# Performance work log

Hardware: AMD Instinct MI355X
Metric: run time of the kernel (lower is better)

## Reference

```python
import jax, jax.numpy as jnp
import numpy as np

N_VERTS = 200000
N_TETS = 800000
FREQ_NUM = 4
SCALE = 1.0
HID = 256
D_IN = 3 + 6 * FREQ_NUM  # 27

_TRI_TABLE = np.array([
    [-1,-1,-1,-1,-1,-1],[1,0,2,-1,-1,-1],[4,0,3,-1,-1,-1],[1,4,2,1,3,4],
    [3,1,5,-1,-1,-1],[2,3,0,2,5,3],[1,4,0,1,5,4],[4,2,5,-1,-1,-1],
    [4,5,2,-1,-1,-1],[4,1,0,4,5,1],[3,2,0,3,5,2],[1,3,5,-1,-1,-1],
    [4,1,2,4,3,1],[3,0,4,-1,-1,-1],[2,0,1,-1,-1,-1],[-1,-1,-1,-1,-1,-1]], dtype=np.int32)
_NUM_TRI = np.array([0,1,1,2,1,2,2,1,1,2,2,1,2,1,1,0], dtype=np.int32)
_BASE_EDGES = np.array([0,1,0,2,0,3,1,2,1,3,2,3], dtype=np.int32)


def _pos_enc(x):
    feats = [x]
    for i in range(FREQ_NUM):
        f = float(2 ** i) * np.pi / SCALE
        feats.append(jnp.sin(f * x))
        feats.append(jnp.cos(f * x))
    return jnp.concatenate(feats, axis=-1)  # [N, 27]


def _mlp_sdf(pos, w0, b0, w1, b1, w2, b2, w3, b3, wf, bf):
    h = jax.nn.relu(_pos_enc(pos) @ w0 + b0)
    for w, b in ((w1, b1), (w2, b2), (w3, b3)):
        h = jax.nn.relu(h @ w + b)
    return (h @ wf + bf)[:, 0]  # [N]


def setup_inputs() -> dict:
    key = jax.random.key(0)
    ks = jax.random.split(key, 12)
    def lin(k, fan_in, shape):
        return jax.random.normal(k, shape, jnp.float32) * (2.0 / fan_in) ** 0.5
    return {
        "pos": jax.random.normal(ks[0], (N_VERTS, 3), jnp.float32),
        "tet_fx4": jax.random.randint(ks[1], (N_TETS, 4), 0, N_VERTS, dtype=jnp.int32),
        "w0": lin(ks[2], D_IN, (D_IN, HID)), "b0": jnp.zeros((HID,), jnp.float32),
        "w1": lin(ks[3], HID, (HID, HID)), "b1": jnp.zeros((HID,), jnp.float32),
        "w2": lin(ks[4], HID, (HID, HID)), "b2": jnp.zeros((HID,), jnp.float32),
        "w3": lin(ks[5], HID, (HID, HID)), "b3": jnp.zeros((HID,), jnp.float32),
        "wf": lin(ks[6], HID, (HID, 1)), "bf": jnp.zeros((1,), jnp.float32),
    }


def reference(pos, tet_fx4, w0, b0, w1, b1, w2, b2, w3, b3, wf, bf):
    # SDF from the positional-encoding MLP (DMTetGeometry)
    sdf = _mlp_sdf(pos, w0, b0, w1, b1, w2, b2, w3, b3, wf, bf)

    # --- marching tetrahedra (DMTet.__call__) ---
    occ = sdf > 0                       # [N]
    occ_fx4 = occ[tet_fx4]              # [F,4]
    occ_sum = occ_fx4.sum(-1)
    valid = (occ_sum > 0) & (occ_sum < 4)
    vt = tet_fx4[valid]                 # [V,4] tets crossed by the surface
    occ_v = occ_fx4[valid]              # [V,4]

    # all 6 edges per valid tet, sorted so (lo, hi)
    e = vt[:, _BASE_EDGES].reshape(-1, 2)                         # [6V,2]
    e = jnp.stack([jnp.minimum(e[:, 0], e[:, 1]),
                   jnp.maximum(e[:, 0], e[:, 1])], axis=1)
    uniq, inv = jnp.unique(e, axis=0, return_inverse=True)        # dedup edges
    inv = inv.reshape(-1)

    # edges whose endpoints straddle the zero level set
    cross = occ[uniq].sum(-1) == 1                                 # [U]
    mapping = jnp.where(cross, jnp.cumsum(cross) - 1, -1)          # compact ids
    idx_map = mapping[inv].reshape(-1, 6)                          # [V,6]
    interp_v = uniq[cross]                                         # [M,2]

    # linear interpolation of crossing vertices along each crossing edge
    p = pos[interp_v]                                              # [M,2,3]
    s = sdf[interp_v]                                              # [M,2]
    denom = s[:, 0] - s[:, 1]                                      # s0 + (-s1)
    verts = (p[:, 0] * (-s[:, 1])[:, None] + p[:, 1] * s[:, 0][:, None]) / denom[:, None]

    # triangle table lookup
    tetindex = (occ_v.astype(jnp.int32) * (2 ** jnp.arange(4, dtype=jnp.int32))).sum(-1)
    ntri = jnp.asarray(_NUM_TRI)[tetindex]
    tri = jnp.asarray(_TRI_TABLE)[tetindex]
    m1 = ntri == 1
    m2 = ntri == 2
    f1 = jnp.take_along_axis(idx_map[m1], tri[m1][:, :3], axis=1).reshape(-1, 3)
    f2 = jnp.take_along_axis(idx_map[m2], tri[m2][:, :6], axis=1).reshape(-1, 3)
    faces = jnp.concatenate([f1, f2], axis=0)
    return verts, faces
```

## Files before the change

kernel.cpp:

```cpp
#include <hip/hip_runtime.h>
#include <cstdint>
#include <cstddef>

#define NV 200000
#define NT 800000
#define ROWS 64
#define MBLK 3125
#define NBLK 3125
#define NSEGS 196
#define PCAP 4096

typedef unsigned int u32;
typedef unsigned long long u64;

typedef __attribute__((ext_vector_type(8))) _Float16 half8;
typedef __attribute__((ext_vector_type(4))) float f32x4;
#define MFMA16F __builtin_amdgcn_mfma_f32_16x16x32_f16

__constant__ int c_tri[16][6] = {
  {-1,-1,-1,-1,-1,-1},{1,0,2,-1,-1,-1},{4,0,3,-1,-1,-1},{1,4,2,1,3,4},
  {3,1,5,-1,-1,-1},{2,3,0,2,5,3},{1,4,0,1,5,4},{4,2,5,-1,-1,-1},
  {4,5,2,-1,-1,-1},{4,1,0,4,5,1},{3,2,0,3,5,2},{1,3,5,-1,-1,-1},
  {4,1,2,4,3,1},{3,0,4,-1,-1,-1},{2,0,1,-1,-1,-1},{-1,-1,-1,-1,-1,-1}};
__constant__ int c_ntri[16] = {0,1,1,2,1,2,2,1,1,2,2,1,2,1,1,0};
__constant__ int c_be[12] = {0,1,0,2,0,3,1,2,1,3,2,3};

__device__ __forceinline__ void split2(float x, _Float16& h, _Float16& m){
  h = (_Float16)x;
  const float r = x - (float)h;
  m = (_Float16)(r * 2048.0f);
}

__global__ void split_weights(const float* __restrict__ w0, const float* __restrict__ w1,
                              const float* __restrict__ w2, const float* __restrict__ w3,
                              _Float16* __restrict__ wp, u32* __restrict__ segcur)
{
  const int idx = blockIdx.x*256 + threadIdx.x;
  if (idx < 256) segcur[idx] = 0u;
  int base, k, n, psz;
  float val;
  if (idx < 8192){
    base = 0; psz = 8192; k = idx >> 8; n = idx & 255;
    val = (k < 27) ? w0[k*256 + n] : 0.f;
  } else {
    int r = idx - 8192;
    const int l = r >> 16;
    r &= 65535;
    k = r >> 8; n = r & 255; psz = 65536;
    base = 16384 + l*131072;
    const float* w = (l==0) ? w1 : (l==1) ? w2 : w3;
    val = w[k*256 + n];
  }
  _Float16 h, m; split2(val, h, m);
  const int c = k >> 5, kk = k & 31;
  const int off = (c*256 + n)*32 + kk;
  wp[base + off] = h;
  wp[base + psz + off] = m;
}

template<int NC, bool LAST>
__device__ __forceinline__ void layer_run(
    const _Float16* __restrict__ Wl, const float* __restrict__ Bv,
    const float* __restrict__ wfv,
    _Float16 (*Af)[ROWS][264], float (*part)[8],
    int lane, int wv)
{
  const int l15 = lane & 15, q = lane >> 4;
  const int col0 = wv * 32;
  f32x4 g0[4][2], g1[4][2];
#pragma unroll
  for (int i=0;i<4;i++)
#pragma unroll
    for (int j=0;j<2;j++){ g0[i][j] = (f32x4){0.f,0.f,0.f,0.f}; g1[i][j] = (f32x4){0.f,0.f,0.f,0.f}; }

  const _Float16* bp = Wl + (u32)((col0 + l15)*32 + q*8);
  half8 bA[2][2], bB[2][2];

  auto loadB = [&](int c, half8 (*dst)[2]){
#pragma unroll
    for (int p=0;p<2;p++)
#pragma unroll
      for (int nt=0;nt<2;nt++)
        dst[p][nt] = *(const half8*)(bp + (p*NC + c)*8192 + nt*512);
  };
  auto compute = [&](int c, const half8 (*bb)[2]){
#pragma unroll
    for (int mt=0;mt<4;mt++){
      const _Float16* ap = &Af[0][mt*16 + l15][c*32 + q*8];
      const half8 ah = *(const half8*)(ap);
      const half8 am = *(const half8*)(ap + ROWS*264);
#pragma unroll
      for (int nt=0;nt<2;nt++){
        g0[mt][nt] = MFMA16F(ah, bb[0][nt], g0[mt][nt], 0,0,0);
        g1[mt][nt] = MFMA16F(ah, bb[1][nt], g1[mt][nt], 0,0,0);
        g1[mt][nt] = MFMA16F(am, bb[0][nt], g1[mt][nt], 0,0,0);
      }
    }
  };

  loadB(0, bA);
  if (NC == 1){
    compute(0, bA);
  } else {
#pragma unroll 1
    for (int ch=0; ch<NC/2; ch++){
      const int c0 = 2*ch;
      loadB(c0+1, bB);
      compute(c0, bA);
      if (c0+2 < NC) loadB(c0+2, bA);
      compute(c0+1, bB);
    }
  }
  __syncthreads();

  const float S = 4.8828125e-4f;
  if (!LAST){
#pragma unroll
    for (int nt=0;nt<2;nt++){
      const int col = col0 + nt*16 + l15;
      const float bias = Bv[col];
#pragma unroll
      for (int mt=0;mt<4;mt++)
#pragma unroll
        for (int reg=0;reg<4;reg++){
          const int row = mt*16 + q*4 + reg;
          const float v = fmaxf(g0[mt][nt][reg] + S*g1[mt][nt][reg] + bias, 0.f);
          _Float16 h,m; split2(v,h,m);
          Af[0][row][col] = h; Af[1][row][col] = m;
        }
    }
  } else {
    float pr[4][4];
#pragma unroll
    for (int mt=0;mt<4;mt++)
#pragma unroll
      for (int reg=0;reg<4;reg++) pr[mt][reg] = 0.f;
#pragma unroll
    for (int nt=0;nt<2;nt++){
      const int col = col0 + nt*16 + l15;
      const float bias = Bv[col];
      const float w = wfv[col];
#pragma unroll
      for (int mt=0;mt<4;mt++)
#pragma unroll
        for (int reg=0;reg<4;reg++)
          pr[mt][reg] += fmaxf(g0[mt][nt][reg] + S*g1[mt][nt][reg] + bias, 0.f) * w;
    }
#pragma unroll
    for (int s=1;s<16;s<<=1)
#pragma unroll
      for (int mt=0;mt<4;mt++)
#pragma unroll
        for (int reg=0;reg<4;reg++)
          pr[mt][reg] += __shfl_xor(pr[mt][reg], s, 64);
    if (l15 == 0){
#pragma unroll
      for (int mt=0;mt<4;mt++)
#pragma unroll
        for (int reg=0;reg<4;reg++)
          part[mt*16 + q*4 + reg][wv] = pr[mt][reg];
    }
  }
  __syncthreads();
}

__global__ __launch_bounds__(512,4) void mlp_mfma(
    const float* __restrict__ pos, const _Float16* __restrict__ wp,
    const float* __restrict__ b0, const float* __restrict__ b1,
    const float* __restrict__ b2, const float* __restrict__ b3,
    const float* __restrict__ wf, const float* __restrict__ bf,
    float* __restrict__ sdf)
{
  __shared__ _Float16 Af[2][ROWS][264];
  __shared__ float part[ROWS][8];
  const int tid = threadIdx.x;
  const int lane = tid & 63, wv = tid >> 6;
  const int row0 = blockIdx.x * ROWS;

#pragma unroll
  for (int it=0; it<4; it++){
    const int idx = it*512 + tid;
    const int r = idx & 63, f = idx >> 6;
    float val = 0.f;
    if (f < 3){
      val = pos[(row0 + r)*3 + f];
    } else if (f < 27){
      const int g = (f-3)/6, rem = (f-3)%6;
      const int d = rem % 3;
      const float x = pos[(row0 + r)*3 + d];
      const float fr = (float)(1 << g) * 3.14159265358979323846f;
      val = (rem < 3) ? sinf(fr*x) : cosf(fr*x);
    }
    _Float16 h,m; split2(val,h,m);
    Af[0][r][f] = h; Af[1][r][f] = m;
  }
  __syncthreads();

  layer_run<1,false>(wp + 0,      b0, nullptr, Af, part, lane, wv);
  layer_run<8,false>(wp + 16384,  b1, nullptr, Af, part, lane, wv);
  layer_run<8,false>(wp + 147456, b2, nullptr, Af, part, lane, wv);
  layer_run<8,true >(wp + 278528, b3, wf,      Af, part, lane, wv);

  if (tid < ROWS){
    float s = 0.f;
#pragma unroll
    for (int w=0; w<8; w++) s += part[tid][w];
    sdf[row0 + tid] = s + bf[0];
  }
}

__device__ __forceinline__ u32 wave_scan_incl(u32 v, int lane){
#pragma unroll
  for (int s=1;s<64;s<<=1){
    const u32 y = __shfl_up(v, s, 64);
    if (lane >= s) v += y;
  }
  return v;
}
__device__ __forceinline__ u32 block_scan_fast(u32 v, u32* sh4, int tid){
  const int lane = tid & 63, wv = tid >> 6;
  const u32 incl = wave_scan_incl(v, lane);
  if (lane == 63) sh4[wv] = incl;
  __syncthreads();
  u32 base = 0;
#pragma unroll
  for (int w=0;w<3;w++) if (w < wv) base += sh4[w];
  return incl + base;
}
__device__ __forceinline__ u64 bscan_u64(u64 v, u64* sh, int tid){
  sh[tid]=v; __syncthreads();
#pragma unroll
  for (int s=1;s<256;s<<=1){
    const u64 y = (tid>=s) ? sh[tid-s] : 0ull;
    __syncthreads();
    sh[tid] += y;
    __syncthreads();
  }
  return sh[tid];
}

__global__ void tet_pairs(const int* __restrict__ tet, const float* __restrict__ sdf,
    unsigned char* __restrict__ codes, u32* __restrict__ tscan, u32* __restrict__ tsum,
    u32* __restrict__ segcur, u64* __restrict__ pairs)
{
  __shared__ u32 sh4[4];
  const int tid = threadIdx.x;
  const int t = blockIdx.x*256 + tid;
  const int4 v = *(const int4*)(&tet[4*t]);
  const int o0 = sdf[v.x] > 0.f;
  const int o1 = sdf[v.y] > 0.f;
  const int o2 = sdf[v.z] > 0.f;
  const int o3 = sdf[v.w] > 0.f;
  const int code = o0 | (o1<<1) | (o2<<2) | (o3<<3);
  codes[t] = (unsigned char)code;
  const int nt = c_ntri[code];
  if (nt > 0){
    const int vv[4] = {v.x, v.y, v.z, v.w};
    const int oc[4] = {o0,o1,o2,o3};
#pragma unroll
    for (int e=0;e<6;e++){
      const int ia = c_be[2*e], ib = c_be[2*e+1];
      if (oc[ia] != oc[ib]){
        const int p = vv[ia], q = vv[ib];
        const int lo = p<q ? p : q, hi = p<q ? q : p;
        const int seg = lo >> 10;
        const u32 slot = atomicAdd(&segcur[seg], 1u);
        if (slot < PCAP)
          pairs[(size_t)seg*PCAP + slot] = ((u64)(u32)lo << 32) | (u32)hi;
      }
    }
  }
  const u32 my = (u32)(nt==1) | ((u32)(nt==2)<<16);
  const u32 incl = block_scan_fast(my, sh4, tid);
  tscan[t] = incl - my;
  if (tid == 255) tsum[blockIdx.x] = incl;
}

__global__ void seg_process(const u64* __restrict__ pairs_in, const u32* __restrict__ segcur,
    u64* __restrict__ uq, u32* __restrict__ ucnt, u32* __restrict__ ucnt_ex,
    u32* __restrict__ usum, const u32* __restrict__ tsum, u64* __restrict__ tsumE,
    u32* __restrict__ meta)
{
  const int tid = threadIdx.x;
  if (blockIdx.x == NSEGS){
    __shared__ u64 sh64[256];
    u64 loc[13]; u64 tot = 0ull;
#pragma unroll
    for (int i=0;i<13;i++){
      const int idx = tid*13 + i;
      const u32 p = (idx < NBLK) ? tsum[idx] : 0u;
      const u64 u = (u64)(p & 0xffffu) | ((u64)(p >> 16) << 32);
      loc[i] = u; tot += u;
    }
    const u64 incl = bscan_u64(tot, sh64, tid);
    u64 run = incl - tot;
#pragma unroll
    for (int i=0;i<13;i++){
      const int idx = tid*13 + i;
      if (idx < NBLK) tsumE[idx] = run;
      run += loc[i];
    }
    if (tid == 255){ meta[0] = (u32)(incl & 0xffffffffull); meta[1] = (u32)(incl >> 32); }
    return;
  }

  __shared__ u64 P[PCAP];
  __shared__ u32 sh4[4];
  __shared__ u32 shbase;
  const int seg = blockIdx.x;
  int n = (int)segcur[seg];
  if (n > PCAP) n = PCAP;
  int np = 1; while (np < n) np <<= 1;

  for (int i=tid; i<np; i+=256)
    P[i] = (i < n) ? pairs_in[(size_t)seg*PCAP + i] : ~0ull;
  if (tid == 0) shbase = 0u;
  __syncthreads();

  for (int k=2; k<=np; k<<=1){
    for (int j=k>>1; j>0; j>>=1){
      for (int i=tid; i<np; i+=256){
        const int ij = i ^ j;
        if (ij > i){
          const u64 a = P[i], b = P[ij];
          const bool up = ((i & k) == 0);
          if ((a > b) == up){ P[i] = b; P[ij] = a; }
        }
      }
      __syncthreads();
    }
  }

  for (int c=0; c<n; c+=256){
    const int i = c + tid;
    u64 key = 0ull; u32 f = 0u;
    if (i < n){
      key = P[i];
      f = (i == 0 || P[i] != P[i-1]) ? 1u : 0u;
    }
    __syncthreads();
    const u32 incl = block_scan_fast(f, sh4, tid);
    const u32 base = shbase;
    if (f) P[base + incl - 1u] = key;
    __syncthreads();
    if (tid == 255) shbase = base + incl;
    __syncthreads();
  }
  const int uc = (int)shbase;

  for (int i=tid; i<uc; i+=256) uq[(size_t)seg*PCAP + i] = P[i];

  const int lo0 = seg << 10;
  for (int c=0; c<1024; c+=256){
    const int lo = lo0 + c + tid;
    if (lo < NV){
      const u64 kl = (u64)(u32)lo << 32;
      const u64 kh = (u64)(u32)(lo+1) << 32;
      int a=0, b=uc;
      while (a < b){ const int m=(a+b)>>1; if (P[m] < kl) a=m+1; else b=m; }
      const int lb = a;
      b = uc;
      while (a < b){ const int m=(a+b)>>1; if (P[m] < kh) a=m+1; else b=m; }
      ucnt_ex[lo] = (u32)lb;
      ucnt[lo] = (u32)(a - lb);
    }
  }
  if (tid == 0) usum[seg] = (u32)uc;
}

__global__ void emit_all(const int* __restrict__ tet, const float* __restrict__ pos,
    const float* __restrict__ sdf, const unsigned char* __restrict__ codes,
    const u32* __restrict__ tscan, const u64* __restrict__ tsumE, const u32* __restrict__ meta,
    const u64* __restrict__ uq, const u32* __restrict__ ucnt, const u32* __restrict__ ucnt_ex,
    const u32* __restrict__ usum, float* __restrict__ out, int out_size)
{
  __shared__ u32 sh4[4];
  __shared__ u32 shu[NSEGS];
  __shared__ u32 shM;
  const int tid = threadIdx.x;
  {
    const u32 v = (tid < NSEGS) ? usum[tid] : 0u;
    const u32 incl = block_scan_fast(v, sh4, tid);
    if (tid < NSEGS) shu[tid] = incl - v;
    if (tid == NSEGS-1) shM = incl;
    __syncthreads();
  }

  if (blockIdx.x < NSEGS){
    const int seg = blockIdx.x;
    const int uc = (int)usum[seg];
    const u32 base = shu[seg];
    for (int i=tid; i<uc; i+=256){
      const u64 key = uq[(size_t)seg*PCAP + i];
      const int lo = (int)(key >> 32);
      const int hi = (int)(key & 0xffffffffull);
      const float s0 = sdf[lo], s1 = sdf[hi];
      const float d = s0 - s1;
      const float vx = (pos[3*lo  ]*(-s1) + pos[3*hi  ]*s0) / d;
      const float vy = (pos[3*lo+1]*(-s1) + pos[3*hi+1]*s0) / d;
      const float vz = (pos[3*lo+2]*(-s1) + pos[3*hi+2]*s0) / d;
      const long long w = 3ll*(long long)(base + (u32)i);
      if (w + 3 <= (long long)out_size){
        out[w] = vx; out[w+1] = vy; out[w+2] = vz;
      }
    }
  } else {
    const int t = (blockIdx.x - NSEGS)*256 + tid;
    const int code = codes[t];
    const int nt = c_ntri[code];
    if (nt == 0) return;
    const u64 tb = tsumE[t>>8];
    const u32 ts = tscan[t];
    const u32 n1e = (u32)(tb & 0xffffffffull) + (ts & 0xffffu);
    const u32 n2e = (u32)(tb >> 32) + (ts >> 16);
    const u32 N1 = meta[0];
    const u32 M  = shM;
    const u32 fb = (nt==1) ? n1e : (N1 + 2u*n2e);
    const int4 v = *(const int4*)(&tet[4*t]);
    const int vv[4] = {v.x, v.y, v.z, v.w};
    for (int r=0;r<nt;r++){
      for (int k=0;k<3;k++){
        const int e = c_tri[code][3*r+k];
        const int ia = c_be[2*e], ib = c_be[2*e+1];
        const int p = vv[ia], q = vv[ib];
        const int lo = p<q ? p : q, hi = p<q ? q : p;
        const int seg = lo >> 10;
        const u32 st = ucnt_ex[lo];
        const int u = (int)ucnt[lo];
        const u64* b = uq + (size_t)seg*PCAP + st;
        int id = -1;
        for (int j=0;j<u;j++){
          if ((int)(b[j] & 0xffffffffull) == hi){ id = (int)(shu[seg] + st) + j; break; }
        }
        const long long w = 3ll*(long long)M + 3ll*(long long)(fb + (u32)r) + k;
        if (w < (long long)out_size && id >= 0) out[w] = (float)id;
      }
    }
  }
}

extern "C" void kernel_launch(void* const* d_in, const int* in_sizes, int n_in,
                              void* d_out, int out_size, void* d_ws, size_t ws_size,
                              hipStream_t stream)
{
  (void)in_sizes; (void)n_in; (void)ws_size;
  const float* pos = (const float*)d_in[0];
  const int*   tet = (const int*)d_in[1];
  const float* w0 = (const float*)d_in[2];
  const float* b0 = (const float*)d_in[3];
  const float* w1 = (const float*)d_in[4];
  const float* b1 = (const float*)d_in[5];
  const float* w2 = (const float*)d_in[6];
  const float* b2 = (const float*)d_in[7];
  const float* w3 = (const float*)d_in[8];
  const float* b3 = (const float*)d_in[9];
  const float* wf = (const float*)d_in[10];
  const float* bf = (const float*)d_in[11];
  float* out = (float*)d_out;
  char* ws = (char*)d_ws;

  float*         sdf   = (float*)(ws + 0);
  unsigned char* codes = (unsigned char*)(ws + 800000);
  u32* tscan   = (u32*)(ws + 1600000);
  u32* tsum    = (u32*)(ws + 4800000);
  u64* tsumE   = (u64*)(ws + 4812800);
  u32* segcur  = (u32*)(ws + 4837888);
  u32* usum    = (u32*)(ws + 4838912);
  u32* meta    = (u32*)(ws + 4839936);
  u32* ucnt    = (u32*)(ws + 4840000);
  u32* ucnt_ex = (u32*)(ws + 5640000);
  _Float16* wp = (_Float16*)(ws + 6440000);
  u64* pairs   = (u64*)(ws + 7259200);

  split_weights<<<800,256,0,stream>>>(w0,w1,w2,w3,wp,segcur);
  mlp_mfma<<<MBLK,512,0,stream>>>(pos,wp,b0,b1,b2,b3,wf,bf,sdf);

  tet_pairs<<<NBLK,256,0,stream>>>(tet,sdf,codes,tscan,tsum,segcur,pairs);
  seg_process<<<NSEGS+1,256,0,stream>>>(pairs,segcur,pairs,ucnt,ucnt_ex,usum,tsum,tsumE,meta);
  emit_all<<<NSEGS+NBLK,256,0,stream>>>(tet,pos,sdf,codes,tscan,tsumE,meta,
                                        pairs,ucnt,ucnt_ex,usum,out,out_size);
}
```

Measured before the change: 455.4 us.

## Replace per-layer block barriers with per-chunk progress flags and ping-pong activation buffers

The MLP kernel now keeps two ping-pong LDS activation buffers. Each wave publishes a per-column-chunk progress flag after writing its outputs, so consumers spin-wait only on the chunk they need instead of hitting a full __syncthreads between layers. Waves also start on staggered K chunks, and the LDS layout is XOR-swizzled to reduce bank conflicts. The aim is to cut barrier stalls between layers. In exchange, the doubled LDS use lowers occupancy (launch bounds drop from 4 to 2 blocks), and the flag polling adds spin overhead.

```diff
diff --git a/kernel.cpp b/kernel.cpp
--- a/kernel.cpp
+++ b/kernel.cpp
@@ -9,6 +9,8 @@
 #define NBLK 3125
 #define NSEGS 196
 #define PCAP 4096
+#define AST 264
+#define PST (ROWS*AST)
 
 typedef unsigned int u32;
 typedef unsigned long long u64;
@@ -58,15 +60,24 @@
   wp[base + psz + off] = m;
 }
 
+__device__ __forceinline__ void waitflag(u32* prog, int c, u32 epoch){
+  if (epoch == 0u) return;
+  while (__hip_atomic_load(&prog[c], __ATOMIC_ACQUIRE, __HIP_MEMORY_SCOPE_WORKGROUP) < epoch)
+    __builtin_amdgcn_s_sleep(1);
+}
+
 template<int NC, bool LAST>
 __device__ __forceinline__ void layer_run(
     const _Float16* __restrict__ Wl, const float* __restrict__ Bv,
     const float* __restrict__ wfv,
-    _Float16 (*Af)[ROWS][264], float (*part)[8],
+    const _Float16* __restrict__ Ain, _Float16* __restrict__ Aout,
+    float (*part)[9], u32* prog, u32 epoch,
     int lane, int wv)
 {
   const int l15 = lane & 15, q = lane >> 4;
   const int col0 = wv * 32;
+  const int rx  = ((l15 >> 3) & 1) << 4;
+  const int q8x = (q * 8) ^ rx;
   f32x4 g0[4][2], g1[4][2];
 #pragma unroll
   for (int i=0;i<4;i++)
@@ -86,9 +97,9 @@
   auto compute = [&](int c, const half8 (*bb)[2]){
 #pragma unroll
     for (int mt=0;mt<4;mt++){
-      const _Float16* ap = &Af[0][mt*16 + l15][c*32 + q*8];
+      const _Float16* ap = Ain + (u32)((mt*16 + l15)*AST + c*32 + q8x);
       const half8 ah = *(const half8*)(ap);
-      const half8 am = *(const half8*)(ap + ROWS*264);
+      const half8 am = *(const half8*)(ap + PST);
 #pragma unroll
       for (int nt=0;nt<2;nt++){
         g0[mt][nt] = MFMA16F(ah, bb[0][nt], g0[mt][nt], 0,0,0);
@@ -98,27 +109,31 @@
     }
   };
 
-  loadB(0, bA);
   if (NC == 1){
+    loadB(0, bA);
     compute(0, bA);
   } else {
+    loadB(wv & (NC-1), bA);
 #pragma unroll 1
     for (int ch=0; ch<NC/2; ch++){
-      const int c0 = 2*ch;
-      loadB(c0+1, bB);
-      compute(c0, bA);
-      if (c0+2 < NC) loadB(c0+2, bA);
-      compute(c0+1, bB);
-    }
-  }
-  __syncthreads();
+      const int cA = (wv + 2*ch)     & (NC-1);
+      const int cB = (wv + 2*ch + 1) & (NC-1);
+      loadB(cB, bB);
+      waitflag(prog, cA, epoch);
+      compute(cA, bA);
+      if (2*ch+2 < NC) loadB((wv + 2*ch + 2) & (NC-1), bA);
+      waitflag(prog, cB, epoch);
+      compute(cB, bB);
+    }
+  }
 
   const float S = 4.8828125e-4f;
   if (!LAST){
+    const int cx = ((q >> 1) & 1) << 4;
 #pragma unroll
     for (int nt=0;nt<2;nt++){
-      const int col = col0 + nt*16 + l15;
-      const float bias = Bv[col];
+      const int colb = ((col0 + nt*16) ^ cx) + l15;
+      const float bias = Bv[col0 + nt*16 + l15];
 #pragma unroll
       for (int mt=0;mt<4;mt++)
 #pragma unroll
@@ -126,9 +141,12 @@
           const int row = mt*16 + q*4 + reg;
           const float v = fmaxf(g0[mt][nt][reg] + S*g1[mt][nt][reg] + bias, 0.f);
           _Float16 h,m; split2(v,h,m);
-          Af[0][row][col] = h; Af[1][row][col] = m;
+          Aout[row*AST + colb] = h;
+          Aout[PST + row*AST + colb] = m;
         }
     }
+    if (lane == 0)
+      __hip_atomic_store(&prog[wv], epoch + 1u, __ATOMIC_RELEASE, __HIP_MEMORY_SCOPE_WORKGROUP);
   } else {
     float pr[4][4];
 #pragma unroll
@@ -161,21 +179,23 @@
           part[mt*16 + q*4 + reg][wv] = pr[mt][reg];
     }
   }
-  __syncthreads();
-}
-
-__global__ __launch_bounds__(512,4) void mlp_mfma(
+}
+
+__global__ __launch_bounds__(512,2) void mlp_mfma(
     const float* __restrict__ pos, const _Float16* __restrict__ wp,
     const float* __restrict__ b0, const float* __restrict__ b1,
     const float* __restrict__ b2, const float* __restrict__ b3,
     const float* __restrict__ wf, const float* __restrict__ bf,
     float* __restrict__ sdf)
 {
-  __shared__ _Float16 Af[2][ROWS][264];
-  __shared__ float part[ROWS][8];
+  __shared__ _Float16 Ab0[2*PST];
+  __shared__ _Float16 Ab1[2*PST];
+  __shared__ float part[ROWS][9];
+  __shared__ u32 prog[8];
   const int tid = threadIdx.x;
   const int lane = tid & 63, wv = tid >> 6;
   const int row0 = blockIdx.x * ROWS;
+  if (tid < 8) prog[tid] = 0u;
 
 #pragma unroll
   for (int it=0; it<4; it++){
@@ -192,14 +212,17 @@
       val = (rem < 3) ? sinf(fr*x) : cosf(fr*x);
     }
     _Float16 h,m; split2(val,h,m);
-    Af[0][r][f] = h; Af[1][r][f] = m;
+    const int fS = f ^ (((r >> 3) & 1) << 4);
+    Ab0[r*AST + fS] = h;
+    Ab0[PST + r*AST + fS] = m;
   }
   __syncthreads();
 
-  layer_run<1,false>(wp + 0,      b0, nullptr, Af, part, lane, wv);
-  layer_run<8,false>(wp + 16384,  b1, nullptr, Af, part, lane, wv);
-  layer_run<8,false>(wp + 147456, b2, nullptr, Af, part, lane, wv);
-  layer_run<8,true >(wp + 278528, b3, wf,      Af, part, lane, wv);
+  layer_run<1,false>(wp + 0,      b0, nullptr, Ab0, Ab1, part, prog, 0u, lane, wv);
+  layer_run<8,false>(wp + 16384,  b1, nullptr, Ab1, Ab0, part, prog, 1u, lane, wv);
+  layer_run<8,false>(wp + 147456, b2, nullptr, Ab0, Ab1, part, prog, 2u, lane, wv);
+  layer_run<8,true >(wp + 278528, b3, wf,      Ab1, nullptr, part, prog, 3u, lane, wv);
+  __syncthreads();
 
   if (tid < ROWS){
     float s = 0.f;
```

Measured after the change: 464.1 us. No clear change (+1.9%).
